# Performance work log

Measured on AMD Instinct MI355X. Metric: run time of the kernel, lower is better.

Reference implementation:

```python
import jax, jax.numpy as jnp
import numpy as np

PAD_ID, SOS_ID, EOS_ID = 0, 1, 2


def setup_inputs() -> dict:
    key = jax.random.key(0)
    ks = jax.random.split(key, 8)
    V, E, H, B = 16000, 256, 512, 8
    s = 0.05  # weight scale to keep softmax well-conditioned
    return {
        "hidden": jax.random.normal(ks[0], (1, B, H), dtype=jnp.float32),
        "embedding": jax.random.normal(ks[1], (V, E), dtype=jnp.float32) * s,
        "w_ih": jax.random.normal(ks[2], (3 * H, E), dtype=jnp.float32) * s,
        "w_hh": jax.random.normal(ks[3], (3 * H, H), dtype=jnp.float32) * s,
        "b_ih": jax.random.normal(ks[4], (3 * H,), dtype=jnp.float32) * s,
        "b_hh": jax.random.normal(ks[5], (3 * H,), dtype=jnp.float32) * s,
        "w_out": jax.random.normal(ks[6], (V, H), dtype=jnp.float32) * s,
        "b_out": jax.random.normal(ks[7], (V,), dtype=jnp.float32) * s,
        "lenseq": 12,
        "k": 5,
    }


def reference(hidden, embedding, w_ih, w_hh, b_ih, b_hh, w_out, b_out, lenseq, k):
    V, E = embedding.shape
    _, B, H = hidden.shape
    dt = hidden.dtype
    pad_onehot = jax.nn.one_hot(PAD_ID, V, dtype=dt)

    def gru_cell(x_emb, h):  # x_emb: (k,B,E), h: (k,B,H); torch nn.GRU gate order r,z,n
        gi = x_emb @ w_ih.T + b_ih
        gh = h @ w_hh.T + b_hh
        i_r, i_z, i_n = jnp.split(gi, 3, axis=-1)
        h_r, h_z, h_n = jnp.split(gh, 3, axis=-1)
        r = jax.nn.sigmoid(i_r + h_r)
        z = jax.nn.sigmoid(i_z + h_z)
        n = jnp.tanh(i_n + r * h_n)
        return (1.0 - z) * n + z * h

    def step(carry, i):
        x, h, prob, res, _ = carry
        done = (x == EOS_ID) | (x == PAD_ID)            # (k,B)
        emb = embedding[x]                               # (k,B,E)
        h_new = gru_cell(emb, h)                         # (k,B,H)
        probs = jax.nn.softmax(h_new @ w_out.T + b_out, axis=-1)  # (k,B,V)
        pred = jnp.where(done[..., None], pad_onehot, probs)
        h = jnp.where(done[..., None], h, h_new)
        res = res.at[:, i].set(pred)                     # store raw pred (pre prob-scaling), as torch.cat copies
        scores = pred * prob[..., None]                  # (k,B,V); prob stays all-ones, faithful to source
        flat = scores.transpose(1, 0, 2).reshape(B, k * V)  # beam-major flatten per batch elem
        _, idx = jax.lax.top_k(flat, k)                  # (B,k)
        beam = (idx // V).T                              # (k,B)
        tok = (idx % V).T                                # (k,B)
        res = jnp.take_along_axis(res, beam[:, None, :, None], axis=0)
        prob = jnp.take_along_axis(prob, beam, axis=0)
        h = jnp.take_along_axis(h, beam[..., None], axis=0)
        return (tok, h, prob, res, pred), None

    x0 = jnp.full((k, B), SOS_ID, dtype=jnp.int32)
    h0 = jnp.broadcast_to(hidden[0], (k, B, H))
    prob0 = jnp.ones((k, B), dtype=dt)
    res0 = jnp.zeros((k, lenseq, B, V), dtype=dt)
    pred0 = jnp.zeros((k, B, V), dtype=dt)

    (x, h, prob, res, pred), _ = jax.lax.scan(step, (x0, h0, prob0, res0, pred0), jnp.arange(lenseq))

    # final top-1 selection per batch element over (k*V) flat scores
    scores = pred * prob[..., None]
    flat = scores.transpose(1, 0, 2).reshape(B, k * V)
    best_beam = jnp.argmax(flat, axis=-1) // V           # (B,)
    out = jnp.take_along_axis(res, best_beam[None, None, :, None], axis=0)[0]  # (lenseq,B,V)
    return out
```

## Files before the change

### kernel.cpp

```cpp
#include <hip/hip_runtime.h>

#define V 16000
#define E 256
#define H 512
#define BB 8
#define T 12


__global__ __launch_bounds__(256) void k0_init(const float* __restrict__ hidden,
                                               float* __restrict__ h_cur,
                                               int* __restrict__ x_cur) {
    int idx = blockIdx.x * 256 + threadIdx.x;
    if (idx < BB * H) {
        h_cur[idx] = hidden[idx];
        if (idx < BB) x_cur[idx] = 1;
    }
}

__global__ __launch_bounds__(256) void kg_gemm(const float* __restrict__ emb_tab,
                                               const float* __restrict__ w_ih,
                                               const float* __restrict__ w_hh,
                                               const int* __restrict__ x_cur,
                                               const float* __restrict__ h_cur,
                                               float* __restrict__ gi_buf,
                                               float* __restrict__ gh_buf) {
    int bid = blockIdx.x;
    bool is_gh = bid < 48;
    int lb = is_gh ? bid : bid - 48;
    int j = lb * 32 + (threadIdx.x >> 3);
    int r = threadIdx.x & 7;

    if (is_gh) {
        const float* w = w_hh + j * H;
        const float* hv = h_cur + r * H;
        float a0 = 0.f, a1 = 0.f;
        for (int k = 0; k < H; k += 4) {
            float4 a = *(const float4*)(w + k);
            float4 b = *(const float4*)(hv + k);
            a0 += a.x * b.x + a.y * b.y;
            a1 += a.z * b.z + a.w * b.w;
        }
        gh_buf[j * BB + r] = a0 + a1;
    } else {
        const float* w = w_ih + j * E;
        const float* ev = emb_tab + (size_t)x_cur[r] * E;
        float a0 = 0.f, a1 = 0.f;
        for (int k = 0; k < E; k += 4) {
            float4 a = *(const float4*)(w + k);
            float4 b = *(const float4*)(ev + k);
            a0 += a.x * b.x + a.y * b.y;
            a1 += a.z * b.z + a.w * b.w;
        }
        gi_buf[j * BB + r] = a0 + a1;
    }
}

__global__ __launch_bounds__(256) void kg_gate(const float* __restrict__ gi_buf,
                                               const float* __restrict__ gh_buf,
                                               const float* __restrict__ b_ih,
                                               const float* __restrict__ b_hh,
                                               const int* __restrict__ x_cur,
                                               const float* __restrict__ h_cur,
                                               float* __restrict__ h_next) {
    int idx = blockIdx.x * 256 + threadIdx.x;
    if (idx >= BB * H) return;
    int r = idx >> 9;
    int j = idx & (H - 1);
    int x = x_cur[r];
    bool done = (x == 2) || (x == 0);
    float ir  = gi_buf[j * BB + r]            + b_ih[j];
    float iz  = gi_buf[(H + j) * BB + r]      + b_ih[H + j];
    float inn = gi_buf[(2 * H + j) * BB + r]  + b_ih[2 * H + j];
    float hr  = gh_buf[j * BB + r]            + b_hh[j];
    float hz  = gh_buf[(H + j) * BB + r]      + b_hh[H + j];
    float hn  = gh_buf[(2 * H + j) * BB + r]  + b_hh[2 * H + j];
    float rg = 1.f / (1.f + __expf(-(ir + hr)));
    float zg = 1.f / (1.f + __expf(-(iz + hz)));
    float ng = tanhf(inn + rg * hn);
    float ho = h_cur[idx];
    float hv = (1.f - zg) * ng + zg * ho;
    h_next[idx] = done ? ho : hv;
}

__global__ __launch_bounds__(256) void klog(const float* __restrict__ w_out,
                                            const float* __restrict__ h,
                                            float* __restrict__ part) {
    int v = blockIdx.x * 256 + threadIdx.x;
    int kq = blockIdx.y;
    if (v >= V) return;
    const float* w = w_out + (size_t)v * H + kq * 128;
    const float* hb = h + kq * 128;
    float acc[8] = {0.f, 0.f, 0.f, 0.f, 0.f, 0.f, 0.f, 0.f};
    for (int k = 0; k < 128; k += 4) {
        float4 w4 = *(const float4*)(w + k);
#pragma unroll
        for (int r = 0; r < 8; r++) {
            float4 h4 = *(const float4*)(hb + r * H + k);
            acc[r] += w4.x * h4.x + w4.y * h4.y + w4.z * h4.z + w4.w * h4.w;
        }
    }
#pragma unroll
    for (int r = 0; r < 8; r++) part[(kq * 8 + r) * V + v] = acc[r];
}

__global__ __launch_bounds__(1024) void ksel(const float* __restrict__ part,
                                             const float* __restrict__ b_out,
                                             float* __restrict__ out_t,
                                             int* __restrict__ x_cur) {
    int b = blockIdx.x;
    int tid = threadIdx.x;
    int x = x_cur[b];
    bool done = (x == 0) || (x == 2);

    if (done) {
        for (int v = tid; v < V; v += 1024) out_t[b * V + v] = (v == 0) ? 1.f : 0.f;
        if (tid == 0) x_cur[b] = 0;
        return;
    }

    __shared__ float rs[1024];
    __shared__ float rv[1024];
    __shared__ int   ri[1024];

    float e[16];
    float sum = 0.f;
#pragma unroll
    for (int i = 0; i < 16; i++) {
        int v = tid + i * 1024;
        if (v < V) {
            float l = part[(0 * 8 + b) * V + v] + part[(1 * 8 + b) * V + v]
                    + part[(2 * 8 + b) * V + v] + part[(3 * 8 + b) * V + v]
                    + b_out[v];
            e[i] = __expf(l);
            sum += e[i];
        } else e[i] = -1.f;
    }
    rs[tid] = sum;
    __syncthreads();
    for (int s = 512; s > 0; s >>= 1) {
        if (tid < s) rs[tid] += rs[tid + s];
        __syncthreads();
    }
    float S = rs[0];
    float inv = 1.f / S;

    float p[16];
    float best = -1.f;
    int bv = 0x7fffffff;
#pragma unroll
    for (int i = 0; i < 16; i++) {
        int v = tid + i * 1024;
        if (v < V) {
            p[i] = e[i] * inv;
            if (p[i] > best || (p[i] == best && v < bv)) { best = p[i]; bv = v; }
        }
    }
    rv[tid] = best; ri[tid] = bv;
    __syncthreads();
    for (int s = 512; s > 0; s >>= 1) {
        if (tid < s) {
            if (rv[tid + s] > rv[tid] ||
                (rv[tid + s] == rv[tid] && ri[tid + s] < ri[tid])) {
                rv[tid] = rv[tid + s]; ri[tid] = ri[tid + s];
            }
        }
        __syncthreads();
    }
    if (tid == 0) x_cur[b] = ri[0];

#pragma unroll
    for (int i = 0; i < 16; i++) {
        int v = tid + i * 1024;
        if (v < V) out_t[b * V + v] = p[i];
    }
}

extern "C" void kernel_launch(void* const* d_in, const int* in_sizes, int n_in,
                              void* d_out, int out_size, void* d_ws, size_t ws_size,
                              hipStream_t stream) {
    (void)in_sizes; (void)n_in; (void)out_size; (void)ws_size;
    const float* hidden    = (const float*)d_in[0];
    const float* embedding = (const float*)d_in[1];
    const float* w_ih      = (const float*)d_in[2];
    const float* w_hh      = (const float*)d_in[3];
    const float* b_ih      = (const float*)d_in[4];
    const float* b_hh      = (const float*)d_in[5];
    const float* w_out     = (const float*)d_in[6];
    const float* b_out     = (const float*)d_in[7];
    float* out = (float*)d_out;

    float* ws   = (float*)d_ws;
    float* hA   = ws;
    float* hB   = hA + BB * H;
    float* gi_buf = hB + BB * H;
    float* gh_buf = gi_buf + 3 * H * BB;
    float* part   = gh_buf + 3 * H * BB;
    int*   x_cur  = (int*)(part + 4 * BB * V);

    k0_init<<<16, 256, 0, stream>>>(hidden, hA, x_cur);
    for (int t = 0; t < T; t++) {
        float* h_cur  = (t & 1) ? hB : hA;
        float* h_next = (t & 1) ? hA : hB;
        kg_gemm<<<96, 256, 0, stream>>>(embedding, w_ih, w_hh, x_cur, h_cur, gi_buf, gh_buf);
        kg_gate<<<16, 256, 0, stream>>>(gi_buf, gh_buf, b_ih, b_hh, x_cur, h_cur, h_next);
        klog<<<dim3(63, 4), 256, 0, stream>>>(w_out, h_next, part);
        ksel<<<8, 1024, 0, stream>>>(part, b_out, out + (size_t)t * BB * V, x_cur);
    }
}
```

Measured before the change: 657.5 us.

## Fuse all decode steps into one persistent kernel with grid barriers

Replaces the 48 per-step kernel launches with a single persistent kernel of 256 blocks that runs all 12 steps, separating phases with software grid barriers built on atomics. GRU gates are computed and applied in the same blocks. Each block keeps its exp(logits) in registers and does local sum and argmax partials, followed by a cross-block reduction, so the logits partial buffer no longer goes through global memory. This removes launch overhead and global round trips. In exchange it relies on all 256 blocks being co-resident and adds spin-barrier latency.

Measured after the change: 1.422 ms. 2.16x slower.

```diff
diff --git a/kernel.cpp b/kernel.cpp
--- a/kernel.cpp
+++ b/kernel.cpp
@@ -5,173 +5,220 @@
 #define H 512
 #define BB 8
 #define T 12
-
-
-__global__ __launch_bounds__(256) void k0_init(const float* __restrict__ hidden,
-                                               float* __restrict__ h_cur,
-                                               int* __restrict__ x_cur) {
+#define NB 256
+#define VPB 63
+
+
+__device__ __forceinline__ float dot4(float4 a, float4 b) {
+    return a.x * b.x + a.y * b.y + a.z * b.z + a.w * b.w;
+}
+
+__global__ __launch_bounds__(256) void kinit(const float* __restrict__ hidden,
+                                             float* __restrict__ hA,
+                                             int* __restrict__ bar) {
     int idx = blockIdx.x * 256 + threadIdx.x;
-    if (idx < BB * H) {
-        h_cur[idx] = hidden[idx];
-        if (idx < BB) x_cur[idx] = 1;
+    if (idx < BB * H) hA[idx] = hidden[idx];
+    if (idx < 2) bar[idx] = 0;
+}
+
+__device__ __forceinline__ void gridbar(int* bar) {
+    __syncthreads();
+    if (threadIdx.x == 0) {
+        __threadfence();
+        int g = __hip_atomic_load(&bar[1], __ATOMIC_RELAXED, __HIP_MEMORY_SCOPE_AGENT);
+        int a = __hip_atomic_fetch_add(&bar[0], 1, __ATOMIC_ACQ_REL, __HIP_MEMORY_SCOPE_AGENT);
+        if (a == NB - 1) {
+            __hip_atomic_store(&bar[0], 0, __ATOMIC_RELAXED, __HIP_MEMORY_SCOPE_AGENT);
+            __hip_atomic_fetch_add(&bar[1], 1, __ATOMIC_RELEASE, __HIP_MEMORY_SCOPE_AGENT);
+        } else {
+            while (__hip_atomic_load(&bar[1], __ATOMIC_RELAXED, __HIP_MEMORY_SCOPE_AGENT) == g)
+                __builtin_amdgcn_s_sleep(1);
+        }
+        __threadfence();
     }
-}
-
-__global__ __launch_bounds__(256) void kg_gemm(const float* __restrict__ emb_tab,
-                                               const float* __restrict__ w_ih,
-                                               const float* __restrict__ w_hh,
-                                               const int* __restrict__ x_cur,
-                                               const float* __restrict__ h_cur,
-                                               float* __restrict__ gi_buf,
-                                               float* __restrict__ gh_buf) {
-    int bid = blockIdx.x;
-    bool is_gh = bid < 48;
-    int lb = is_gh ? bid : bid - 48;
-    int j = lb * 32 + (threadIdx.x >> 3);
-    int r = threadIdx.x & 7;
-
-    if (is_gh) {
-        const float* w = w_hh + j * H;
-        const float* hv = h_cur + r * H;
-        float a0 = 0.f, a1 = 0.f;
-        for (int k = 0; k < H; k += 4) {
-            float4 a = *(const float4*)(w + k);
-            float4 b = *(const float4*)(hv + k);
-            a0 += a.x * b.x + a.y * b.y;
-            a1 += a.z * b.z + a.w * b.w;
-        }
-        gh_buf[j * BB + r] = a0 + a1;
-    } else {
-        const float* w = w_ih + j * E;
-        const float* ev = emb_tab + (size_t)x_cur[r] * E;
-        float a0 = 0.f, a1 = 0.f;
-        for (int k = 0; k < E; k += 4) {
-            float4 a = *(const float4*)(w + k);
-            float4 b = *(const float4*)(ev + k);
-            a0 += a.x * b.x + a.y * b.y;
-            a1 += a.z * b.z + a.w * b.w;
-        }
-        gi_buf[j * BB + r] = a0 + a1;
-    }
-}
-
-__global__ __launch_bounds__(256) void kg_gate(const float* __restrict__ gi_buf,
-                                               const float* __restrict__ gh_buf,
-                                               const float* __restrict__ b_ih,
-                                               const float* __restrict__ b_hh,
-                                               const int* __restrict__ x_cur,
-                                               const float* __restrict__ h_cur,
-                                               float* __restrict__ h_next) {
-    int idx = blockIdx.x * 256 + threadIdx.x;
-    if (idx >= BB * H) return;
-    int r = idx >> 9;
-    int j = idx & (H - 1);
-    int x = x_cur[r];
-    bool done = (x == 2) || (x == 0);
-    float ir  = gi_buf[j * BB + r]            + b_ih[j];
-    float iz  = gi_buf[(H + j) * BB + r]      + b_ih[H + j];
-    float inn = gi_buf[(2 * H + j) * BB + r]  + b_ih[2 * H + j];
-    float hr  = gh_buf[j * BB + r]            + b_hh[j];
-    float hz  = gh_buf[(H + j) * BB + r]      + b_hh[H + j];
-    float hn  = gh_buf[(2 * H + j) * BB + r]  + b_hh[2 * H + j];
-    float rg = 1.f / (1.f + __expf(-(ir + hr)));
-    float zg = 1.f / (1.f + __expf(-(iz + hz)));
-    float ng = tanhf(inn + rg * hn);
-    float ho = h_cur[idx];
-    float hv = (1.f - zg) * ng + zg * ho;
-    h_next[idx] = done ? ho : hv;
-}
-
-__global__ __launch_bounds__(256) void klog(const float* __restrict__ w_out,
-                                            const float* __restrict__ h,
-                                            float* __restrict__ part) {
-    int v = blockIdx.x * 256 + threadIdx.x;
-    int kq = blockIdx.y;
-    if (v >= V) return;
-    const float* w = w_out + (size_t)v * H + kq * 128;
-    const float* hb = h + kq * 128;
-    float acc[8] = {0.f, 0.f, 0.f, 0.f, 0.f, 0.f, 0.f, 0.f};
-    for (int k = 0; k < 128; k += 4) {
-        float4 w4 = *(const float4*)(w + k);
+    __syncthreads();
+}
+
+__global__ __launch_bounds__(256, 4) void kmain(
+    const float* __restrict__ emb_tab,
+    const float* __restrict__ w_ih,
+    const float* __restrict__ w_hh,
+    const float* __restrict__ b_ih,
+    const float* __restrict__ b_hh,
+    const float* __restrict__ w_out,
+    const float* __restrict__ b_out,
+    float* __restrict__ hA,
+    float* __restrict__ hB,
+    float* __restrict__ psum,
+    float* __restrict__ pval,
+    int* __restrict__ pidx,
+    int* __restrict__ bar,
+    float* __restrict__ out)
+{
+    const int blk = blockIdx.x, tid = threadIdx.x;
+
+    __shared__ float s_part[64 * 24];
+    __shared__ float s_v[256];
+    __shared__ float s_av[256];
+    __shared__ int   s_ai[256];
+    __shared__ float s_S[BB];
+    __shared__ int   s_Xn[BB];
+    __shared__ int   s_X[BB];
+
+    if (tid < BB) s_X[tid] = 1;
+    __syncthreads();
+
+    const int r   = tid & 7;
+    const int vl0 = tid >> 3;
+    const int vl1 = vl0 + 32;
+    const int v_0 = blk * VPB + vl0;
+    const int v_1 = blk * VPB + vl1;
+    const bool ok0 = (v_0 < V);
+    const bool ok1 = (vl1 < VPB) && (v_1 < V);
+
+    float e0 = 0.f, e1 = 0.f;
+
+    for (int t = 0; t < T; t++) {
+        const float* h_cur = (t & 1) ? hB : hA;
+        float*       h_nxt = (t & 1) ? hA : hB;
+
+        if (blk < 64) {
+            const int p  = tid >> 2;
+            const int q  = tid & 3;
+            const int jl = p >> 3;
+            const int ar = p & 7;
+            const int j  = blk * 8 + jl;
+            const int xr = s_X[ar];
+            const float* erow = emb_tab + (size_t)xr * E;
+            const float* hrow = h_cur + ar * H;
+            float gir = 0.f, giz = 0.f, gin = 0.f, ghr = 0.f, ghz = 0.f, ghn = 0.f;
+            {
+                const float* w0 = w_ih + (size_t)j * E;
+                const float* w1 = w0 + (size_t)H * E;
+                const float* w2 = w1 + (size_t)H * E;
+                const int k0 = q * (E / 4);
+                for (int k = k0; k < k0 + E / 4; k += 4) {
+                    float4 ev = *(const float4*)(erow + k);
+                    gir += dot4(*(const float4*)(w0 + k), ev);
+                    giz += dot4(*(const float4*)(w1 + k), ev);
+                    gin += dot4(*(const float4*)(w2 + k), ev);
+                }
+            }
+            {
+                const float* w0 = w_hh + (size_t)j * H;
+                const float* w1 = w0 + (size_t)H * H;
+                const float* w2 = w1 + (size_t)H * H;
+                const int k0 = q * (H / 4);
+                for (int k = k0; k < k0 + H / 4; k += 4) {
+                    float4 hv = *(const float4*)(hrow + k);
+                    ghr += dot4(*(const float4*)(w0 + k), hv);
+                    ghz += dot4(*(const float4*)(w1 + k), hv);
+                    ghn += dot4(*(const float4*)(w2 + k), hv);
+                }
+            }
+            float* sp = s_part + p * 24;
+            sp[0 * 4 + q] = gir; sp[1 * 4 + q] = giz; sp[2 * 4 + q] = gin;
+            sp[3 * 4 + q] = ghr; sp[4 * 4 + q] = ghz; sp[5 * 4 + q] = ghn;
+        }
+        __syncthreads();
+        if (blk < 64 && (tid & 3) == 0) {
+            const int p  = tid >> 2;
+            const int jl = p >> 3;
+            const int ar = p & 7;
+            const int j  = blk * 8 + jl;
+            const float* sp = s_part + p * 24;
+            float Gir = sp[0]  + sp[1]  + sp[2]  + sp[3];
+            float Giz = sp[4]  + sp[5]  + sp[6]  + sp[7];
+            float Gin = sp[8]  + sp[9]  + sp[10] + sp[11];
+            float Ghr = sp[12] + sp[13] + sp[14] + sp[15];
+            float Ghz = sp[16] + sp[17] + sp[18] + sp[19];
+            float Ghn = sp[20] + sp[21] + sp[22] + sp[23];
+            float ir  = Gir + b_ih[j],         hr_ = Ghr + b_hh[j];
+            float iz  = Giz + b_ih[H + j],     hz  = Ghz + b_hh[H + j];
+            float inn = Gin + b_ih[2 * H + j], hn  = Ghn + b_hh[2 * H + j];
+            float rg = 1.f / (1.f + __expf(-(ir + hr_)));
+            float zg = 1.f / (1.f + __expf(-(iz + hz)));
+            float ng = tanhf(inn + rg * hn);
+            float ho = h_cur[ar * H + j];
+            int xr = s_X[ar];
+            bool dn = (xr == 0) || (xr == 2);
+            h_nxt[ar * H + j] = dn ? ho : ((1.f - zg) * ng + zg * ho);
+        }
+        gridbar(bar);
+
+        {
+            const float* hrow = h_nxt + r * H;
+            const float* w0 = w_out + (size_t)(ok0 ? v_0 : 0) * H;
+            const float* w1 = w_out + (size_t)(ok1 ? v_1 : 0) * H;
+            float a0 = 0.f, a1 = 0.f;
+            for (int k = 0; k < H; k += 4) {
+                float4 hv = *(const float4*)(hrow + k);
+                a0 += dot4(*(const float4*)(w0 + k), hv);
+                a1 += dot4(*(const float4*)(w1 + k), hv);
+            }
+            e0 = __expf(a0 + b_out[ok0 ? v_0 : 0]);
+            e1 = __expf(a1 + b_out[ok1 ? v_1 : 0]);
+
+            float ls = 0.f, bv = -1.f; int bi = 0x7fffffff;
+            if (ok0) { ls += e0; if (e0 > bv || (e0 == bv && v_0 < bi)) { bv = e0; bi = v_0; } }
+            if (ok1) { ls += e1; if (e1 > bv || (e1 == bv && v_1 < bi)) { bv = e1; bi = v_1; } }
+            s_v[tid] = ls; s_av[tid] = bv; s_ai[tid] = bi;
+        }
+        __syncthreads();
+        for (int s = 128; s >= 8; s >>= 1) {
+            if (tid < s) {
+                s_v[tid] += s_v[tid + s];
+                float ov = s_av[tid + s]; int oi = s_ai[tid + s];
+                if (ov > s_av[tid] || (ov == s_av[tid] && oi < s_ai[tid])) {
+                    s_av[tid] = ov; s_ai[tid] = oi;
+                }
+            }
+            __syncthreads();
+        }
+        if (tid < 8) {
+            psum[blk * 8 + tid] = s_v[tid];
+            pval[blk * 8 + tid] = s_av[tid];
+            pidx[blk * 8 + tid] = s_ai[tid];
+        }
+        gridbar(bar);
+
+        {
+            const int wv = tid >> 6, lane = tid & 63;
+            for (int rr = 0; rr < 2; rr++) {
+                const int rw = wv * 2 + rr;
+                float s = psum[lane * 8 + rw] + psum[(lane + 64) * 8 + rw]
+                        + psum[(lane + 128) * 8 + rw] + psum[(lane + 192) * 8 + rw];
+                float bv = pval[lane * 8 + rw]; int bi = pidx[lane * 8 + rw];
 #pragma unroll
-        for (int r = 0; r < 8; r++) {
-            float4 h4 = *(const float4*)(hb + r * H + k);
-            acc[r] += w4.x * h4.x + w4.y * h4.y + w4.z * h4.z + w4.w * h4.w;
-        }
-    }
-#pragma unroll
-    for (int r = 0; r < 8; r++) part[(kq * 8 + r) * V + v] = acc[r];
-}
-
-__global__ __launch_bounds__(1024) void ksel(const float* __restrict__ part,
-                                             const float* __restrict__ b_out,
-                                             float* __restrict__ out_t,
-                                             int* __restrict__ x_cur) {
-    int b = blockIdx.x;
-    int tid = threadIdx.x;
-    int x = x_cur[b];
-    bool done = (x == 0) || (x == 2);
-
-    if (done) {
-        for (int v = tid; v < V; v += 1024) out_t[b * V + v] = (v == 0) ? 1.f : 0.f;
-        if (tid == 0) x_cur[b] = 0;
-        return;
-    }
-
-    __shared__ float rs[1024];
-    __shared__ float rv[1024];
-    __shared__ int   ri[1024];
-
-    float e[16];
-    float sum = 0.f;
-#pragma unroll
-    for (int i = 0; i < 16; i++) {
-        int v = tid + i * 1024;
-        if (v < V) {
-            float l = part[(0 * 8 + b) * V + v] + part[(1 * 8 + b) * V + v]
-                    + part[(2 * 8 + b) * V + v] + part[(3 * 8 + b) * V + v]
-                    + b_out[v];
-            e[i] = __expf(l);
-            sum += e[i];
-        } else e[i] = -1.f;
-    }
-    rs[tid] = sum;
-    __syncthreads();
-    for (int s = 512; s > 0; s >>= 1) {
-        if (tid < s) rs[tid] += rs[tid + s];
-        __syncthreads();
-    }
-    float S = rs[0];
-    float inv = 1.f / S;
-
-    float p[16];
-    float best = -1.f;
-    int bv = 0x7fffffff;
-#pragma unroll
-    for (int i = 0; i < 16; i++) {
-        int v = tid + i * 1024;
-        if (v < V) {
-            p[i] = e[i] * inv;
-            if (p[i] > best || (p[i] == best && v < bv)) { best = p[i]; bv = v; }
-        }
-    }
-    rv[tid] = best; ri[tid] = bv;
-    __syncthreads();
-    for (int s = 512; s > 0; s >>= 1) {
-        if (tid < s) {
-            if (rv[tid + s] > rv[tid] ||
-                (rv[tid + s] == rv[tid] && ri[tid + s] < ri[tid])) {
-                rv[tid] = rv[tid + s]; ri[tid] = ri[tid + s];
-            }
-        }
-        __syncthreads();
-    }
-    if (tid == 0) x_cur[b] = ri[0];
-
-#pragma unroll
-    for (int i = 0; i < 16; i++) {
-        int v = tid + i * 1024;
-        if (v < V) out_t[b * V + v] = p[i];
+                for (int c = 1; c < 4; c++) {
+                    float ov = pval[(lane + 64 * c) * 8 + rw];
+                    int   oi = pidx[(lane + 64 * c) * 8 + rw];
+                    if (ov > bv || (ov == bv && oi < bi)) { bv = ov; bi = oi; }
+                }
+                for (int m = 1; m < 64; m <<= 1) {
+                    s += __shfl_xor(s, m, 64);
+                    float ov = __shfl_xor(bv, m, 64);
+                    int   oi = __shfl_xor(bi, m, 64);
+                    if (ov > bv || (ov == bv && oi < bi)) { bv = ov; bi = oi; }
+                }
+                if (lane == 0) { s_S[rw] = s; s_Xn[rw] = bi; }
+            }
+        }
+        __syncthreads();
+        {
+            float* out_t = out + (size_t)t * BB * V;
+            int xr = s_X[r];
+            bool dn = (xr == 0) || (xr == 2);
+            float inv = 1.f / s_S[r];
+            if (ok0) out_t[r * V + v_0] = dn ? ((v_0 == 0) ? 1.f : 0.f) : e0 * inv;
+            if (ok1) out_t[r * V + v_1] = dn ? ((v_1 == 0) ? 1.f : 0.f) : e1 * inv;
+        }
+        __syncthreads();
+        if (tid < 8) {
+            int xo = s_X[tid];
+            s_X[tid] = ((xo == 0) || (xo == 2)) ? 0 : s_Xn[tid];
+        }
+        __syncthreads();
     }
 }
 
@@ -192,18 +239,12 @@
     float* ws   = (float*)d_ws;
     float* hA   = ws;
     float* hB   = hA + BB * H;
-    float* gi_buf = hB + BB * H;
-    float* gh_buf = gi_buf + 3 * H * BB;
-    float* part   = gh_buf + 3 * H * BB;
-    int*   x_cur  = (int*)(part + 4 * BB * V);
-
-    k0_init<<<16, 256, 0, stream>>>(hidden, hA, x_cur);
-    for (int t = 0; t < T; t++) {
-        float* h_cur  = (t & 1) ? hB : hA;
-        float* h_next = (t & 1) ? hA : hB;
-        kg_gemm<<<96, 256, 0, stream>>>(embedding, w_ih, w_hh, x_cur, h_cur, gi_buf, gh_buf);
-        kg_gate<<<16, 256, 0, stream>>>(gi_buf, gh_buf, b_ih, b_hh, x_cur, h_cur, h_next);
-        klog<<<dim3(63, 4), 256, 0, stream>>>(w_out, h_next, part);
-        ksel<<<8, 1024, 0, stream>>>(part, b_out, out + (size_t)t * BB * V, x_cur);
-    }
-}
+    float* psum = hB + BB * H;
+    float* pval = psum + NB * 8;
+    int*   pidx = (int*)(pval + NB * 8);
+    int*   bar  = pidx + NB * 8;
+
+    kinit<<<16, 256, 0, stream>>>(hidden, hA, bar);
+    kmain<<<NB, 256, 0, stream>>>(embedding, w_ih, w_hh, b_ih, b_hh, w_out, b_out,
+                                  hA, hB, psum, pval, pidx, bar, out);
+}
```
